# Performance work log

Hardware: AMD Instinct MI355X
Metric: run time of the kernel (lower is better)

## Reference

```python
import jax, jax.numpy as jnp
import numpy as np

MIN_SCALE = 1e-3
TEMPERATURE = 1.5


def setup_inputs() -> dict:
    key = jax.random.key(0)
    ks = jax.random.split(key, 9)
    B, S, D, R, C = 1024, 64, 512, 16, 1000
    s = 1.0 / np.sqrt(D)  # scale weights for numerical sanity
    return {
        "features": jax.random.normal(ks[0], (B, D), jnp.float32),
        "W_cov": jax.random.normal(ks[1], (D * R, D), jnp.float32) * s,
        "b_cov": jnp.zeros((D * R,), jnp.float32),
        "W_diag": jax.random.normal(ks[2], (D, D), jnp.float32) * s,
        "b_diag": jnp.zeros((D,), jnp.float32),
        "W_cls": jax.random.normal(ks[3], (C, D), jnp.float32) * s,
        "b_cls": jnp.zeros((C,), jnp.float32),
        "noise_diag": jax.random.normal(ks[4], (B, S, D), jnp.float32),
        "noise_lr": jax.random.normal(ks[5], (B, S, R), jnp.float32),
    }


def reference(features, W_cov, b_cov, W_diag, b_diag, W_cls, b_cls, noise_diag, noise_lr):
    B, D = features.shape
    R = noise_lr.shape[-1]
    # Linear(D -> D*R), reshape to (B, D, R) (row-major, matches torch .reshape)
    low_rank_cov = (features @ W_cov.T + b_cov).reshape(B, D, R)
    # diagonal std: softplus(Linear(D->D)) + min_scale
    diagonal_std = jax.nn.softplus(features @ W_diag.T + b_diag) + MIN_SCALE
    # samples: low-rank part + diagonal part, both (B, S, D)
    samples = (
        jnp.einsum("bdr,bsr->bsd", low_rank_cov, noise_lr)
        + diagonal_std[:, None, :] * noise_diag
    )
    pre_logits = features[:, None, :] + samples  # (B, S, D)
    logits = pre_logits @ W_cls.T + b_cls  # (B, S, C)
    return logits / TEMPERATURE
```

## Files before the change

### kernel.cpp

```cpp
#include <hip/hip_runtime.h>
#include <math.h>

typedef __attribute__((ext_vector_type(8))) short bf16x8;
typedef __attribute__((ext_vector_type(4))) float f32x4;
typedef __attribute__((ext_vector_type(4))) unsigned short u16x4;

__device__ inline unsigned short f2bf(float f) {
    union { float f; unsigned u; } v; v.f = f;
    unsigned r = v.u + 0x7FFFu + ((v.u >> 16) & 1u);
    return (unsigned short)(r >> 16);
}
__device__ inline float bf2f(unsigned short h) {
    union { unsigned u; float f; } v; v.u = ((unsigned)h) << 16;
    return v.f;
}

__device__ inline void load_lds16(const void* g, void* l) {
    __builtin_amdgcn_global_load_lds(
        (const __attribute__((address_space(1))) unsigned int*)g,
        (__attribute__((address_space(3))) unsigned int*)l,
        16, 0, 0);
}

__global__ __launch_bounds__(256) void convert_all(
    const float* __restrict__ sA, unsigned short* __restrict__ dA, long nA,
    const float* __restrict__ sB, unsigned short* __restrict__ dB, long nB,
    const float* __restrict__ sC, unsigned short* __restrict__ dC, long nC,
    const float* __restrict__ sD, unsigned short* __restrict__ dD, long nDs, long nDd)
{
    long i = ((long)blockIdx.x * 256 + threadIdx.x) * 4;
    const float* s; unsigned short* d; long nsrc;
    if (i < nA)              { s = sA + i; d = dA + i; nsrc = nA - i; }
    else if ((i -= nA) < nB) { s = sB + i; d = dB + i; nsrc = nB - i; }
    else if ((i -= nB) < nC) { s = sC + i; d = dC + i; nsrc = nC - i; }
    else if ((i -= nC) < nDd){ s = sD + i; d = dD + i; nsrc = nDs - i; }
    else return;
    float4 v = make_float4(0.f, 0.f, 0.f, 0.f);
    if (nsrc >= 4) v = *(const float4*)s;
    u16x4 o;
    o[0] = f2bf(v.x); o[1] = f2bf(v.y); o[2] = f2bf(v.z); o[3] = f2bf(v.w);
    *(u16x4*)d = o;
}

__global__ __launch_bounds__(256) void gemm1_k(
    const unsigned short* __restrict__ A, const unsigned short* __restrict__ Bm,
    const float* __restrict__ bias0, const float* __restrict__ bias1,
    unsigned short* __restrict__ out0, float* __restrict__ out1,
    int M, int Npad, int K, int nsplit)
{
    __shared__ __align__(16) unsigned short As[64 * 64];
    __shared__ __align__(16) unsigned short Bs[128 * 64];

    const int nblk = Npad >> 7;
    const int mt = blockIdx.x / nblk;
    const int nt = blockIdx.x - mt * nblk;
    const int m0 = mt << 6;
    const int n0 = nt << 7;

    const int tid  = threadIdx.x;
    const int lane = tid & 63;
    const int wid  = tid >> 6;
    const int quad = lane >> 4;
    const int l15  = lane & 15;
    const int l7   = l15 & 7;
    const int lrow = lane >> 3;
    const int lcol = ((lane & 7) ^ lrow) << 3;

    const unsigned short* Ab = A  + (size_t)(m0 + lrow) * K + lcol;
    const unsigned short* Bb = Bm + (size_t)(n0 + lrow) * K + lcol;

    f32x4 acc[4][2];
    #pragma unroll
    for (int i = 0; i < 4; ++i)
        #pragma unroll
        for (int j = 0; j < 2; ++j)
            acc[i][j] = f32x4{0.f, 0.f, 0.f, 0.f};

    for (int kt = 0; kt < K; kt += 64) {
        __syncthreads();
        #pragma unroll
        for (int i = 0; i < 6; ++i) {
            const int r0 = wid * 48 + i * 8;
            if (r0 < 64) load_lds16(Ab + (size_t)r0 * K + kt, &As[r0 * 64]);
            else         load_lds16(Bb + (size_t)(r0 - 64) * K + kt, &Bs[(r0 - 64) * 64]);
        }
        __syncthreads();

        #pragma unroll
        for (int kk = 0; kk < 64; kk += 32) {
            const int kq = kk >> 3;
            bf16x8 af[4], bfv[2];
            #pragma unroll
            for (int mi = 0; mi < 4; ++mi)
                af[mi] = *(const bf16x8*)&As[(mi * 16 + l15) * 64
                                             + (((kq + quad) ^ l7) << 3)];
            #pragma unroll
            for (int ni = 0; ni < 2; ++ni)
                bfv[ni] = *(const bf16x8*)&Bs[(wid * 32 + ni * 16 + l15) * 64
                                              + (((kq + quad) ^ l7) << 3)];
            #pragma unroll
            for (int mi = 0; mi < 4; ++mi)
                #pragma unroll
                for (int ni = 0; ni < 2; ++ni)
                    acc[mi][ni] = __builtin_amdgcn_mfma_f32_16x16x32_bf16(
                        bfv[ni], af[mi], acc[mi][ni], 0, 0, 0);
        }
    }

    if (n0 < nsplit) {
        #pragma unroll
        for (int ni = 0; ni < 2; ++ni) {
            const int nb = n0 + wid * 32 + ni * 16 + (quad << 2);
            const float4 bv = *(const float4*)&bias0[nb];
            #pragma unroll
            for (int mi = 0; mi < 4; ++mi) {
                const int m = m0 + mi * 16 + l15;
                u16x4 ov;
                ov[0] = f2bf(acc[mi][ni][0] + bv.x);
                ov[1] = f2bf(acc[mi][ni][1] + bv.y);
                ov[2] = f2bf(acc[mi][ni][2] + bv.z);
                ov[3] = f2bf(acc[mi][ni][3] + bv.w);
                *(u16x4*)&out0[(size_t)m * nsplit + nb] = ov;
            }
        }
    } else {
        const int ld1 = Npad - nsplit;
        #pragma unroll
        for (int ni = 0; ni < 2; ++ni) {
            const int nb = n0 + wid * 32 + ni * 16 + (quad << 2) - nsplit;
            const float4 bv = *(const float4*)&bias1[nb];
            #pragma unroll
            for (int mi = 0; mi < 4; ++mi) {
                const int m = m0 + mi * 16 + l15;
                f32x4 v;
                #pragma unroll
                for (int r = 0; r < 4; ++r) {
                    float x = acc[mi][ni][r] + ((const float*)&bv)[r];
                    float sp = (x > 20.f) ? x : log1pf(expf(x));
                    v[r] = sp + 1e-3f;
                }
                *(f32x4*)&out1[(size_t)m * ld1 + nb] = v;
            }
        }
    }
}

template <bool SWZ>
__global__ __launch_bounds__(512, 4) void gemm2_k(
    const unsigned short* __restrict__ A, const unsigned short* __restrict__ Bm,
    const float* __restrict__ bias0, float* __restrict__ out,
    int M, int Npad, int Nreal, int K)
{
    __shared__ __align__(16) unsigned short As[128 * 64];
    __shared__ __align__(16) unsigned short Bs[256 * 64];

    const int nblk = Npad >> 8;
    int mt, nt;
    if constexpr (SWZ) {
        const int per = (M >> 7) >> 3;
        const int x = blockIdx.x & 7;
        const int j = blockIdx.x >> 3;
        const int jm = j / nblk;
        mt = x * per + jm;
        nt = j - jm * nblk;
    } else {
        mt = blockIdx.x / nblk;
        nt = blockIdx.x - mt * nblk;
    }
    const int m0 = mt << 7;
    const int n0 = nt << 8;

    const int tid  = threadIdx.x;
    const int lane = tid & 63;
    const int wid  = tid >> 6;
    const int wmh  = wid >> 2;
    const int wnq  = wid & 3;
    const int quad = lane >> 4;
    const int l15  = lane & 15;
    const int l7   = l15 & 7;
    const int lrow = lane >> 3;
    const int lcol = ((lane & 7) ^ lrow) << 3;

    const unsigned short* Ab = A  + (size_t)(m0 + lrow) * K + lcol;
    const unsigned short* Bb = Bm + (size_t)(n0 + lrow) * K + lcol;

    f32x4 acc[4][4];
    #pragma unroll
    for (int i = 0; i < 4; ++i)
        #pragma unroll
        for (int j = 0; j < 4; ++j)
            acc[i][j] = f32x4{0.f, 0.f, 0.f, 0.f};

    for (int kt = 0; kt < K; kt += 64) {
        __syncthreads();
        #pragma unroll
        for (int i = 0; i < 6; ++i) {
            const int r0 = wid * 48 + i * 8;
            if (r0 < 128) load_lds16(Ab + (size_t)r0 * K + kt, &As[r0 * 64]);
            else          load_lds16(Bb + (size_t)(r0 - 128) * K + kt, &Bs[(r0 - 128) * 64]);
        }
        __syncthreads();

        #pragma unroll
        for (int kk = 0; kk < 64; kk += 32) {
            const int kq = kk >> 3;
            bf16x8 af[4], bfv[4];
            #pragma unroll
            for (int mi = 0; mi < 4; ++mi)
                af[mi] = *(const bf16x8*)&As[(wmh * 64 + mi * 16 + l15) * 64
                                             + (((kq + quad) ^ l7) << 3)];
            #pragma unroll
            for (int ni = 0; ni < 4; ++ni)
                bfv[ni] = *(const bf16x8*)&Bs[(wnq * 64 + ni * 16 + l15) * 64
                                              + (((kq + quad) ^ l7) << 3)];
            #pragma unroll
            for (int mi = 0; mi < 4; ++mi)
                #pragma unroll
                for (int ni = 0; ni < 4; ++ni)
                    acc[mi][ni] = __builtin_amdgcn_mfma_f32_16x16x32_bf16(
                        bfv[ni], af[mi], acc[mi][ni], 0, 0, 0);
        }
    }

    #pragma unroll
    for (int ni = 0; ni < 4; ++ni) {
        const int nb = n0 + wnq * 64 + ni * 16 + (quad << 2);
        if (nb < Nreal) {
            const float4 bv = *(const float4*)&bias0[nb];
            #pragma unroll
            for (int mi = 0; mi < 4; ++mi) {
                const int m = m0 + wmh * 64 + mi * 16 + l15;
                f32x4 v;
                v[0] = (acc[mi][ni][0] + bv.x) * (1.0f / 1.5f);
                v[1] = (acc[mi][ni][1] + bv.y) * (1.0f / 1.5f);
                v[2] = (acc[mi][ni][2] + bv.z) * (1.0f / 1.5f);
                v[3] = (acc[mi][ni][3] + bv.w) * (1.0f / 1.5f);
                __builtin_nontemporal_store(v, (f32x4*)&out[(size_t)m * Nreal + nb]);
            }
        }
    }
}

__global__ __launch_bounds__(256) void sample_kernel(
    const float* __restrict__ features, const unsigned short* __restrict__ lr_cov,
    const float* __restrict__ diag, const float* __restrict__ nz_lr,
    const float* __restrict__ nz_diag, unsigned short* __restrict__ pre,
    int S, int D)
{
    const int tid = threadIdx.x;
    const int b   = blockIdx.x;
    const int sh  = tid >> 7;
    const int t   = tid & 127;
    const int d0  = t << 2;

    __shared__ __align__(16) float snz[64 * 16];
    ((float4*)snz)[tid] = ((const float4*)(nz_lr + (size_t)b * S * 16))[tid];

    float4 f  = *(const float4*)(features + (size_t)b * D + d0);
    float4 dg = *(const float4*)(diag + (size_t)b * D + d0);
    float L[4][16];
    const unsigned short* lp = lr_cov + (size_t)b * D * 16 + (size_t)d0 * 16;
    #pragma unroll
    for (int j = 0; j < 4; ++j) {
        bf16x8 a = *(const bf16x8*)(lp + j * 16);
        bf16x8 c = *(const bf16x8*)(lp + j * 16 + 8);
        #pragma unroll
        for (int r = 0; r < 8; ++r) {
            L[j][r]     = bf2f((unsigned short)a[r]);
            L[j][8 + r] = bf2f((unsigned short)c[r]);
        }
    }
    __syncthreads();

    const int s0 = sh * (S >> 1);
    const float* ndp = nz_diag + (size_t)b * S * D + (size_t)s0 * D + d0;
    unsigned short* pp = pre + (size_t)b * S * D + (size_t)s0 * D + d0;
    const int SH = S >> 1;
    for (int s = 0; s < SH; s += 4) {
        f32x4 nd[4];
        #pragma unroll
        for (int j = 0; j < 4; ++j)
            nd[j] = __builtin_nontemporal_load((const f32x4*)(ndp + (size_t)(s + j) * D));
        float o[4][4];
        #pragma unroll
        for (int j = 0; j < 4; ++j) {
            o[j][0] = f.x + dg.x * nd[j][0];
            o[j][1] = f.y + dg.y * nd[j][1];
            o[j][2] = f.z + dg.z * nd[j][2];
            o[j][3] = f.w + dg.w * nd[j][3];
        }
        #pragma unroll
        for (int r = 0; r < 16; ++r) {
            #pragma unroll
            for (int j = 0; j < 4; ++j) {
                const float zv = snz[(s0 + s + j) * 16 + r];
                o[j][0] += L[0][r] * zv;
                o[j][1] += L[1][r] * zv;
                o[j][2] += L[2][r] * zv;
                o[j][3] += L[3][r] * zv;
            }
        }
        #pragma unroll
        for (int j = 0; j < 4; ++j) {
            u16x4 ov;
            ov[0] = f2bf(o[j][0]); ov[1] = f2bf(o[j][1]);
            ov[2] = f2bf(o[j][2]); ov[3] = f2bf(o[j][3]);
            *(u16x4*)(pp + (size_t)(s + j) * D) = ov;
        }
    }
}

extern "C" void kernel_launch(void* const* d_in, const int* in_sizes, int n_in,
                              void* d_out, int out_size, void* d_ws, size_t ws_size,
                              hipStream_t stream)
{
    const float* features = (const float*)d_in[0];
    const float* W_cov    = (const float*)d_in[1];
    const float* b_cov    = (const float*)d_in[2];
    const float* W_diag   = (const float*)d_in[3];
    const float* b_diag   = (const float*)d_in[4];
    const float* W_cls    = (const float*)d_in[5];
    const float* b_cls    = (const float*)d_in[6];
    const float* nz_diag  = (const float*)d_in[7];
    const float* nz_lr    = (const float*)d_in[8];

    const int D    = in_sizes[4];
    const int DR   = in_sizes[2];
    const int B    = in_sizes[0] / D;
    const int S    = in_sizes[7] / (B * D);
    const int C    = in_sizes[6];
    const int M    = B * S;
    const int Cpad = (C + 255) & ~255;
    const int Ncat = DR + D;

    char* ws = (char*)d_ws;
    unsigned short* lrcov = (unsigned short*)ws;
    float*          diag  = (float*)(ws + (size_t)B * DR * 2);
    unsigned short* wclsb = (unsigned short*)((char*)diag + (size_t)B * D * 4);
    char* X = (char*)wclsb + (size_t)Cpad * D * 2;
    unsigned short* featb = (unsigned short*)X;
    unsigned short* wcatb = featb + (size_t)B * D;
    unsigned short* pre   = (unsigned short*)X;

    {
        long n1 = (long)DR * D;
        long n2 = (long)D * D;
        long n3 = (long)B * D;
        long n4s = (long)C * D, n4d = (long)Cpad * D;
        long total = n1 + n2 + n3 + n4d;
        convert_all<<<dim3((unsigned)(total / 1024)), 256, 0, stream>>>(
            W_cov, wcatb, n1,
            W_diag, wcatb + n1, n2,
            features, featb, n3,
            W_cls, wclsb, n4s, n4d);
    }

    gemm1_k<<<dim3((B / 64) * (Ncat / 128)), 256, 0, stream>>>(
        featb, wcatb, b_cov, b_diag, lrcov, diag, B, Ncat, D, DR);

    sample_kernel<<<dim3(B), 256, 0, stream>>>(
        features, lrcov, diag, nz_lr, nz_diag, pre, S, D);

    gemm2_k<true><<<dim3((M / 128) * (Cpad / 256)), 512, 0, stream>>>(
        pre, wclsb, b_cls, (float*)d_out, M, Cpad, C, D);
}
```

Measured before the change: 564.6 us.

## Restructure classifier GEMM into full-width row strips with resident A tile

Replaces the 128x256 tiled classifier GEMM with a kernel where each block computes a 32-row strip across all padded classes (1024), loading the whole 32x512 A strip into LDS once and streaming 1024x64 B tiles per k-step. This removes repeated A reads across N tiles and the swizzled tile scheduling. In exchange, LDS use grows to 160KB per block, which drops occupancy to one block per CU, and each block reads the full W_cls every time, so B traffic from L2 rises substantially.

Result: slower. 599.1 us (+6.1%).

```diff
diff --git a/kernel.cpp b/kernel.cpp
--- a/kernel.cpp
+++ b/kernel.cpp
@@ -145,91 +145,77 @@
     }
 }
 
-template <bool SWZ>
-__global__ __launch_bounds__(512, 4) void gemm2_k(
+__global__ __launch_bounds__(512) void gemm2_strip(
     const unsigned short* __restrict__ A, const unsigned short* __restrict__ Bm,
     const float* __restrict__ bias0, float* __restrict__ out,
     int M, int Npad, int Nreal, int K)
 {
-    __shared__ __align__(16) unsigned short As[128 * 64];
-    __shared__ __align__(16) unsigned short Bs[256 * 64];
-
-    const int nblk = Npad >> 8;
-    int mt, nt;
-    if constexpr (SWZ) {
-        const int per = (M >> 7) >> 3;
-        const int x = blockIdx.x & 7;
-        const int j = blockIdx.x >> 3;
-        const int jm = j / nblk;
-        mt = x * per + jm;
-        nt = j - jm * nblk;
-    } else {
-        mt = blockIdx.x / nblk;
-        nt = blockIdx.x - mt * nblk;
-    }
-    const int m0 = mt << 7;
-    const int n0 = nt << 8;
-
+    __shared__ __align__(16) unsigned short As[32 * 512];
+    __shared__ __align__(16) unsigned short Bs[1024 * 64];
+
+    const int m0   = blockIdx.x << 5;
     const int tid  = threadIdx.x;
     const int lane = tid & 63;
     const int wid  = tid >> 6;
-    const int wmh  = wid >> 2;
-    const int wnq  = wid & 3;
     const int quad = lane >> 4;
     const int l15  = lane & 15;
     const int l7   = l15 & 7;
     const int lrow = lane >> 3;
     const int lcol = ((lane & 7) ^ lrow) << 3;
 
-    const unsigned short* Ab = A  + (size_t)(m0 + lrow) * K + lcol;
-    const unsigned short* Bb = Bm + (size_t)(n0 + lrow) * K + lcol;
-
-    f32x4 acc[4][4];
-    #pragma unroll
-    for (int i = 0; i < 4; ++i)
-        #pragma unroll
-        for (int j = 0; j < 4; ++j)
+    #pragma unroll
+    for (int i = 0; i < 4; ++i) {
+        const int row = wid * 4 + i;
+        load_lds16(A + (size_t)(m0 + row) * K + ((lane ^ (row & 7)) << 3),
+                   &As[row * 512]);
+    }
+
+    f32x4 acc[2][8];
+    #pragma unroll
+    for (int i = 0; i < 2; ++i)
+        #pragma unroll
+        for (int j = 0; j < 8; ++j)
             acc[i][j] = f32x4{0.f, 0.f, 0.f, 0.f};
 
     for (int kt = 0; kt < K; kt += 64) {
         __syncthreads();
         #pragma unroll
-        for (int i = 0; i < 6; ++i) {
-            const int r0 = wid * 48 + i * 8;
-            if (r0 < 128) load_lds16(Ab + (size_t)r0 * K + kt, &As[r0 * 64]);
-            else          load_lds16(Bb + (size_t)(r0 - 128) * K + kt, &Bs[(r0 - 128) * 64]);
+        for (int i = 0; i < 16; ++i) {
+            const int rb = wid * 128 + i * 8;
+            load_lds16(Bm + (size_t)(rb + lrow) * K + kt + lcol, &Bs[rb * 64]);
         }
         __syncthreads();
 
         #pragma unroll
         for (int kk = 0; kk < 64; kk += 32) {
-            const int kq = kk >> 3;
-            bf16x8 af[4], bfv[4];
-            #pragma unroll
-            for (int mi = 0; mi < 4; ++mi)
-                af[mi] = *(const bf16x8*)&As[(wmh * 64 + mi * 16 + l15) * 64
-                                             + (((kq + quad) ^ l7) << 3)];
-            #pragma unroll
-            for (int ni = 0; ni < 4; ++ni)
-                bfv[ni] = *(const bf16x8*)&Bs[(wnq * 64 + ni * 16 + l15) * 64
-                                              + (((kq + quad) ^ l7) << 3)];
-            #pragma unroll
-            for (int mi = 0; mi < 4; ++mi)
+            bf16x8 af[2], bfv[8];
+            const int kcA = (kt + kk) >> 3;
+            const int kcB = kk >> 3;
+            #pragma unroll
+            for (int mi = 0; mi < 2; ++mi)
+                af[mi] = *(const bf16x8*)&As[(mi * 16 + l15) * 512
+                                             + (((kcA + quad) ^ l7) << 3)];
+            #pragma unroll
+            for (int ni = 0; ni < 8; ++ni)
+                bfv[ni] = *(const bf16x8*)&Bs[(wid * 128 + ni * 16 + l15) * 64
+                                              + (((kcB + quad) ^ l7) << 3)];
+            #pragma unroll
+            for (int mi = 0; mi < 2; ++mi)
                 #pragma unroll
-                for (int ni = 0; ni < 4; ++ni)
+                for (int ni = 0; ni < 8; ++ni)
                     acc[mi][ni] = __builtin_amdgcn_mfma_f32_16x16x32_bf16(
                         bfv[ni], af[mi], acc[mi][ni], 0, 0, 0);
         }
     }
 
     #pragma unroll
-    for (int ni = 0; ni < 4; ++ni) {
-        const int nb = n0 + wnq * 64 + ni * 16 + (quad << 2);
+    for (int ni = 0; ni < 8; ++ni) {
+        const int nb = wid * 128 + ni * 16 + (quad << 2);
         if (nb < Nreal) {
             const float4 bv = *(const float4*)&bias0[nb];
             #pragma unroll
-            for (int mi = 0; mi < 4; ++mi) {
-                const int m = m0 + wmh * 64 + mi * 16 + l15;
+            for (int mi = 0; mi < 2; ++mi) {
+                const int m = m0 + mi * 16 + l15;
                 f32x4 v;
                 v[0] = (acc[mi][ni][0] + bv.x) * (1.0f / 1.5f);
                 v[1] = (acc[mi][ni][1] + bv.y) * (1.0f / 1.5f);
@@ -361,6 +347,6 @@
     sample_kernel<<<dim3(B), 256, 0, stream>>>(
         features, lrcov, diag, nz_lr, nz_diag, pre, S, D);
 
-    gemm2_k<true><<<dim3((M / 128) * (Cpad / 256)), 512, 0, stream>>>(
+    gemm2_strip<<<dim3(M / 32), 512, 0, stream>>>(
         pre, wclsb, b_cls, (float*)d_out, M, Cpad, C, D);
 }
```
